# Kernel optimization log

Hardware: AMD Instinct MI355X
Metric: run time of the kernel (lower is better)

The kernel has to match this reference:

```python
import jax, jax.numpy as jnp
import numpy as np

N = 8192
C_IN = 512
C_INTER = 128  # in_channels // unit_nums = 512 // 4


def setup_inputs() -> dict:
    key = jax.random.key(0)
    ks = jax.random.split(key, 6)
    x = jax.random.normal(ks[0], (N, C_IN), dtype=jnp.float32)
    # Linear weights init: normal(0, 0.01); biases zero. Stored as [in, out].
    Wg = 0.01 * jax.random.normal(ks[1], (C_IN, C_INTER), dtype=jnp.float32)
    Wt = 0.01 * jax.random.normal(ks[2], (C_IN, C_INTER), dtype=jnp.float32)
    Wp = 0.01 * jax.random.normal(ks[3], (C_IN, C_INTER), dtype=jnp.float32)
    bg = jnp.zeros((C_INTER,), dtype=jnp.float32)
    bt = jnp.zeros((C_INTER,), dtype=jnp.float32)
    bp = jnp.zeros((C_INTER,), dtype=jnp.float32)
    # 1x1 conv weight (1, 2*C_INTER, 1, 1) flattened: first half hits theta, second half phi
    wcat = 0.01 * jax.random.normal(ks[4], (2 * C_INTER,), dtype=jnp.float32)
    return {"x": x, "Wg": Wg, "bg": bg, "Wt": Wt, "bt": bt, "Wp": Wp, "bp": bp, "wcat": wcat}


def reference(x, Wg, bg, Wt, bt, Wp, bp, wcat):
    n = x.shape[0]
    g_x = x @ Wg + bg          # [N, C_inter]
    theta = x @ Wt + bt        # [N, C_inter]
    phi = x @ Wp + bp          # [N, C_inter]
    c = theta.shape[1]
    # 1x1 conv over cat([theta_i, phi_j]) == w1.theta_i + w2.phi_j (outer sum), then ReLU
    a = theta @ wcat[:c]       # [N]
    b = phi @ wcat[c:]         # [N]
    f = jax.nn.relu(a[:, None] + b[None, :])  # [N, N]
    z = (f / n) @ g_x          # [N, C_inter]
    return z
```

## Files before the change

kernel.cpp:

```cpp
#include <hip/hip_runtime.h>

#define C_IN   512
#define C_INT  128
#define NBUCK  8192
#define SEG    32
#define NSEG   256

typedef short short8 __attribute__((ext_vector_type(8)));
typedef float floatx4 __attribute__((ext_vector_type(4)));


__device__ __forceinline__ int bucket_of(float v, float bmin, float inv_w) {
    float fk = (v - bmin) * inv_w;
    fk = fminf(fmaxf(fk, 0.f), (float)(NBUCK - 1));
    return (int)fk;
}

__device__ __forceinline__ short bf16rnd(float v) {
    unsigned u = __float_as_uint(v);
    return (short)((u + 0x7fffu + ((u >> 16) & 1u)) >> 16);
}


__global__ __launch_bounds__(256) void prep_kernel(
        const float* __restrict__ Wt, const float* __restrict__ Wp,
        const float* __restrict__ Wg, const float* __restrict__ wcat,
        const float* __restrict__ bt, const float* __restrict__ bp,
        float* __restrict__ ut, float* __restrict__ up, float* __restrict__ scal,
        unsigned short* __restrict__ WgT) {
    int t = threadIdx.x, bk = blockIdx.x;
    if (bk < 16) {
        const float* W  = (bk < 8) ? Wt : Wp;
        const float* wv = wcat + ((bk < 8) ? 0 : C_INT);
        float* dst      = (bk < 8) ? ut : up;
        int k = (bk & 7) * 64 + (t >> 2);
        int q = t & 3;
        const float4* row = (const float4*)(W + (size_t)k * C_INT);
        const float4* cv4 = (const float4*)wv;
        float s = 0.f;
        #pragma unroll
        for (int i = 0; i < 8; ++i) {
            float4 a = row[q * 8 + i];
            float4 c = cv4[q * 8 + i];
            s += a.x * c.x + a.y * c.y + a.z * c.z + a.w * c.w;
        }
        s += __shfl_xor(s, 1);
        s += __shfl_xor(s, 2);
        if (q == 0) dst[k] = s;
    } else if (bk == 16) {
        float sumsq = 0.f;
        const float4* w2v = (const float4*)(wcat + C_INT);
        for (int r = 0; r < 2; ++r) {
            int k = t * 2 + r;
            const float4* row = (const float4*)(Wp + (size_t)k * C_INT);
            float d = 0.f;
            #pragma unroll
            for (int i = 0; i < 32; ++i) {
                float4 a4 = row[i]; float4 c4 = w2v[i];
                d += a4.x * c4.x + a4.y * c4.y + a4.z * c4.z + a4.w * c4.w;
            }
            sumsq += d * d;
        }
        float s1p = (t < C_INT) ? bt[t] * wcat[t] : 0.f;
        float s2p = (t < C_INT) ? bp[t] * wcat[C_INT + t] : 0.f;
        for (int off = 32; off; off >>= 1) {
            s1p   += __shfl_down(s1p, off);
            s2p   += __shfl_down(s2p, off);
            sumsq += __shfl_down(sumsq, off);
        }
        __shared__ float red[12];
        int w = t >> 6, lane = t & 63;
        if (lane == 0) { red[w] = s1p; red[4 + w] = s2p; red[8 + w] = sumsq; }
        __syncthreads();
        if (t == 0) {
            float s0 = red[0] + red[1] + red[2] + red[3];
            float s1 = red[4] + red[5] + red[6] + red[7];
            float sq = red[8] + red[9] + red[10] + red[11];
            float sigma = sqrtf(sq);
            scal[0] = s0; scal[1] = s1;
            if (sigma > 1e-20f) {
                scal[2] = s1 - 8.f * sigma;
                scal[3] = (float)NBUCK / (16.f * sigma);
            } else {
                scal[2] = s1 - 1.f; scal[3] = 0.f;
            }
        }
    } else {
        __shared__ float tile[64][132];
        int kb = (bk - 17) * 64;
        #pragma unroll
        for (int it = 0; it < 8; ++it) {
            int idx = it * 256 + t;
            int r = idx >> 5, c4 = idx & 31;
            *(float4*)&tile[r][c4 * 4] =
                ((const float4*)(Wg + (size_t)(kb + r) * C_INT))[c4];
        }
        __syncthreads();
        int n = t & 127, kc = (t >> 7) * 32;
        unsigned pk[16];
        #pragma unroll
        for (int i = 0; i < 16; ++i) {
            unsigned lo = (unsigned short)bf16rnd(tile[kc + 2 * i][n]);
            unsigned hi = (unsigned short)bf16rnd(tile[kc + 2 * i + 1][n]);
            pk[i] = lo | (hi << 16);
        }
        uint4* dst = (uint4*)(WgT + (size_t)n * C_IN + kb + kc);
        #pragma unroll
        for (int i2 = 0; i2 < 4; ++i2) dst[i2] = *(uint4*)&pk[i2 * 4];
    }
}


#define RSTR 66

__global__ __launch_bounds__(256) void gemm_mfma(
        const float* __restrict__ x, const unsigned short* __restrict__ WgT,
        const float* __restrict__ bg,
        const float* __restrict__ ut, const float* __restrict__ up,
        const float* __restrict__ scal,
        _Float16* __restrict__ g, float* __restrict__ a, float* __restrict__ b) {
    __shared__ float red[3][36][RSTR];
    int tid = threadIdx.x;
    int lane = tid & 63, wv = tid >> 6;
    int i0 = blockIdx.x * 16;
    int m = lane & 15, q = lane >> 4;
    floatx4 accg[8] = {};
    floatx4 accab = {};
    const float* xrow = x + (size_t)(i0 + m) * C_IN + q * 8;
    const float* absrc = (m == 0) ? ut : up;
    #pragma unroll
    for (int ks = 0; ks < 4; ++ks) {
        int k0 = (wv * 4 + ks) * 32;
        float4 f0 = *(const float4*)(xrow + k0);
        float4 f1 = *(const float4*)(xrow + k0 + 4);
        short8 af;
        af[0] = bf16rnd(f0.x); af[1] = bf16rnd(f0.y);
        af[2] = bf16rnd(f0.z); af[3] = bf16rnd(f0.w);
        af[4] = bf16rnd(f1.x); af[5] = bf16rnd(f1.y);
        af[6] = bf16rnd(f1.z); af[7] = bf16rnd(f1.w);
        short8 abf = {};
        if (m < 2) {
            float4 u0 = *(const float4*)(absrc + k0 + q * 8);
            float4 u1 = *(const float4*)(absrc + k0 + q * 8 + 4);
            abf[0] = bf16rnd(u0.x); abf[1] = bf16rnd(u0.y);
            abf[2] = bf16rnd(u0.z); abf[3] = bf16rnd(u0.w);
            abf[4] = bf16rnd(u1.x); abf[5] = bf16rnd(u1.y);
            abf[6] = bf16rnd(u1.z); abf[7] = bf16rnd(u1.w);
        }
        accab = __builtin_amdgcn_mfma_f32_16x16x32_bf16(af, abf, accab, 0, 0, 0);
        #pragma unroll
        for (int f = 0; f < 8; ++f) {
            short8 bfr = *(const short8*)(WgT + (size_t)(f * 16 + m) * C_IN + k0 + q * 8);
            accg[f] = __builtin_amdgcn_mfma_f32_16x16x32_bf16(af, bfr, accg[f], 0, 0, 0);
        }
    }
    if (wv) {
        #pragma unroll
        for (int f = 0; f < 8; ++f)
            #pragma unroll
            for (int r = 0; r < 4; ++r)
                red[wv - 1][f * 4 + r][lane] = accg[f][r];
        #pragma unroll
        for (int r = 0; r < 4; ++r)
            red[wv - 1][32 + r][lane] = accab[r];
    }
    __syncthreads();
    if (wv == 0) {
        #pragma unroll
        for (int w = 0; w < 3; ++w) {
            #pragma unroll
            for (int f = 0; f < 8; ++f)
                #pragma unroll
                for (int r = 0; r < 4; ++r)
                    accg[f][r] += red[w][f * 4 + r][lane];
            #pragma unroll
            for (int r = 0; r < 4; ++r)
                accab[r] += red[w][32 + r][lane];
        }
        #pragma unroll
        for (int f = 0; f < 8; ++f) {
            int col = f * 16 + m;
            float bgv = bg[col];
            #pragma unroll
            for (int r = 0; r < 4; ++r) {
                int row = i0 + q * 4 + r;
                g[(size_t)row * C_INT + col] = (_Float16)(accg[f][r] + bgv);
            }
        }
        if (m < 2) {
            float off = m ? scal[1] : scal[0];
            float* dst = m ? b : a;
            #pragma unroll
            for (int r = 0; r < 4; ++r) dst[i0 + q * 4 + r] = accab[r] + off;
        }
    }
}


__global__ __launch_bounds__(1024) void sort_kernel(
        const float* __restrict__ b, const float* __restrict__ scal,
        unsigned* __restrict__ offs_g, unsigned short* __restrict__ perm_g,
        float* __restrict__ bsort_g) {
    __shared__ unsigned oh[NBUCK / 2];
    __shared__ unsigned cur[NBUCK / 2];
    __shared__ unsigned short ls[8192];
    __shared__ unsigned wtu[16];
    int t = threadIdx.x, lane = t & 63, wv = t >> 6;
    #pragma unroll
    for (int r = 0; r < 4; ++r) { oh[t + r * 1024] = 0u; cur[t + r * 1024] = 0u; }
    __syncthreads();
    float bmin = scal[2], inv_w = scal[3];
    int kb[8];
    #pragma unroll
    for (int r = 0; r < 8; ++r) {
        int j = t + r * 1024;
        kb[r] = bucket_of(b[j], bmin, inv_w);
        atomicAdd(&oh[kb[r] >> 1], (kb[r] & 1) ? 0x10000u : 1u);
    }
    __syncthreads();
    unsigned h[8], p = 0;
    #pragma unroll
    for (int w = 0; w < 4; ++w) {
        unsigned word = oh[t * 4 + w];
        p += word & 0xffffu;  h[w * 2]     = p;
        p += word >> 16;      h[w * 2 + 1] = p;
    }
    unsigned v = p;
    #pragma unroll
    for (int d = 1; d < 64; d <<= 1) {
        unsigned u = __shfl_up(v, d);
        if (lane >= d) v += u;
    }
    if (lane == 63) wtu[wv] = v;
    __syncthreads();
    if (t < 16) {
        unsigned w = wtu[t];
        #pragma unroll
        for (int d = 1; d < 16; d <<= 1) {
            unsigned u = __shfl_up(w, d);
            if (t >= d) w += u;
        }
        wtu[t] = w;
    }
    __syncthreads();
    unsigned base = (v - p) + (wv ? wtu[wv - 1] : 0u);
    #pragma unroll
    for (int w = 0; w < 4; ++w) {
        unsigned lo = base + h[w * 2], hi = base + h[w * 2 + 1];
        oh[t * 4 + w] = lo | (hi << 16);
        offs_g[t * 8 + w * 2 + 1] = lo;
        offs_g[t * 8 + w * 2 + 2] = hi;
    }
    if (t == 0) offs_g[0] = 0u;
    __syncthreads();
    #pragma unroll
    for (int r = 0; r < 8; ++r) {
        int j = t + r * 1024;
        int k = kb[r];
        unsigned st = 0u;
        if (k > 0) {
            unsigned word = oh[(k - 1) >> 1];
            st = ((k - 1) & 1) ? (word >> 16) : (word & 0xffffu);
        }
        unsigned old = atomicAdd(&cur[k >> 1], (k & 1) ? 0x10000u : 1u);
        unsigned pos = (k & 1) ? (old >> 16) : (old & 0xffffu);
        ls[st + pos] = (unsigned short)j;
    }
    __syncthreads();
    #pragma unroll
    for (int r = 0; r < 8; ++r) {
        int e = t + r * 1024;
        int j = ls[e];
        perm_g[e] = (unsigned short)j;
        bsort_g[e] = b[j];
    }
}


__global__ __launch_bounds__(128) void segsum_kernel(
        const _Float16* __restrict__ g, const unsigned short* __restrict__ perm,
        const float* __restrict__ bsort,
        float* __restrict__ seg1, float* __restrict__ seg2) {
    __shared__ int pj[SEG];
    __shared__ float pb[SEG];
    int s = blockIdx.x, t = threadIdx.x;
    if (t < SEG) { pj[t] = perm[s * SEG + t]; pb[t] = bsort[s * SEG + t]; }
    __syncthreads();
    float a1 = 0.f, a2 = 0.f;
    #pragma unroll
    for (int e = 0; e < SEG; ++e) {
        float gv = (float)g[(size_t)pj[e] * C_INT + t];
        a1 += gv; a2 += pb[e] * gv;
    }
    seg1[s * C_INT + t] = a1;
    seg2[s * C_INT + t] = a2;
}


__global__ __launch_bounds__(128) void expand_kernel(
        const _Float16* __restrict__ g, const unsigned short* __restrict__ perm,
        const float* __restrict__ bsort,
        const float* __restrict__ seg1, const float* __restrict__ seg2,
        float* __restrict__ Pr1, float* __restrict__ Pr2) {
    __shared__ int pj[SEG];
    __shared__ float pb[SEG];
    int s = blockIdx.x, t = threadIdx.x;
    if (t < SEG) { pj[t] = perm[s * SEG + t]; pb[t] = bsort[s * SEG + t]; }
    __syncthreads();
    float r1 = 0.f, r2 = 0.f;
    for (int s2 = s + 1; s2 < NSEG; ++s2) {
        r1 += seg1[s2 * C_INT + t];
        r2 += seg2[s2 * C_INT + t];
    }
    #pragma unroll
    for (int e = SEG - 1; e >= 0; --e) {
        float gv = (float)g[(size_t)pj[e] * C_INT + t];
        r1 += gv; r2 += pb[e] * gv;
        size_t idx = (size_t)(s * SEG + e) * C_INT + t;
        Pr1[idx] = r1; Pr2[idx] = r2;
    }
    if (s == NSEG - 1) {
        Pr1[(size_t)8192 * C_INT + t] = 0.f;
        Pr2[(size_t)8192 * C_INT + t] = 0.f;
    }
}


__global__ __launch_bounds__(128) void out_kernel(
        const float* __restrict__ a, const float* __restrict__ scal,
        const _Float16* __restrict__ g,
        const unsigned* __restrict__ offs, const unsigned short* __restrict__ perm,
        const float* __restrict__ bsort,
        const float* __restrict__ Pr1, const float* __restrict__ Pr2,
        float* __restrict__ out, float inv_n) {
    __shared__ int pj[128];
    __shared__ float pb[128];
    int i = blockIdx.x, c = threadIdx.x;
    float ai = a[i], thr = -ai;
    float bmin = scal[2], inv_w = scal[3];
    int ki = bucket_of(thr, bmin, inv_w);
    unsigned e0 = offs[ki], e1 = offs[ki + 1];
    size_t base = (size_t)e1 * C_INT + c;
    float acc = ai * Pr1[base] + Pr2[base];
    for (unsigned be = e0; be < e1; be += 128) {
        unsigned cnt = min(128u, e1 - be);
        if ((unsigned)c < cnt) { pj[c] = perm[be + c]; pb[c] = bsort[be + c]; }
        __syncthreads();
        for (unsigned r = 0; r < cnt; ++r) {
            float bj = pb[r];
            if (bj > thr)
                acc += (ai + bj) * (float)g[(size_t)pj[r] * C_INT + c];
        }
        __syncthreads();
    }
    out[(size_t)i * C_INT + c] = acc * inv_n;
}


extern "C" void kernel_launch(void* const* d_in, const int* in_sizes, int n_in,
                              void* d_out, int out_size, void* d_ws, size_t ws_size,
                              hipStream_t stream) {
    const float* x    = (const float*)d_in[0];
    const float* Wg   = (const float*)d_in[1];
    const float* bg   = (const float*)d_in[2];
    const float* Wt   = (const float*)d_in[3];
    const float* bt   = (const float*)d_in[4];
    const float* Wp   = (const float*)d_in[5];
    const float* bp   = (const float*)d_in[6];
    const float* wcat = (const float*)d_in[7];
    float* out = (float*)d_out;
    int n = in_sizes[0] / C_IN;

    char* w = (char*)d_ws;
    size_t off = 0;
    auto alloc = [&](size_t bytes) -> void* {
        void* p = w + off;
        off += (bytes + 255) & ~(size_t)255;
        return p;
    };
    float*          ut    = (float*)alloc(C_IN * 4);
    float*          up    = (float*)alloc(C_IN * 4);
    float*          scal  = (float*)alloc(16);
    float*          a     = (float*)alloc((size_t)n * 4);
    float*          b     = (float*)alloc((size_t)n * 4);
    unsigned*       offs  = (unsigned*)alloc((size_t)(NBUCK + 1) * 4);
    unsigned short* perm  = (unsigned short*)alloc((size_t)n * 2);
    float*          bsort = (float*)alloc((size_t)n * 4);
    _Float16*       g     = (_Float16*)alloc((size_t)n * C_INT * 2);
    unsigned short* WgT   = (unsigned short*)alloc((size_t)C_INT * C_IN * 2);
    float*          seg1  = (float*)alloc((size_t)NSEG * C_INT * 4);
    float*          seg2  = (float*)alloc((size_t)NSEG * C_INT * 4);
    float*          Pr1   = (float*)alloc((size_t)(n + 1) * C_INT * 4);
    float*          Pr2   = (float*)alloc((size_t)(n + 1) * C_INT * 4);

    prep_kernel<<<25, 256, 0, stream>>>(Wt, Wp, Wg, wcat, bt, bp, ut, up, scal, WgT);
    gemm_mfma<<<n / 16, 256, 0, stream>>>(x, WgT, bg, ut, up, scal, g, a, b);
    sort_kernel<<<1, 1024, 0, stream>>>(b, scal, offs, perm, bsort);
    segsum_kernel<<<NSEG, 128, 0, stream>>>(g, perm, bsort, seg1, seg2);
    expand_kernel<<<NSEG, 128, 0, stream>>>(g, perm, bsort, seg1, seg2, Pr1, Pr2);
    out_kernel<<<n, 128, 0, stream>>>(a, scal, g, offs, perm, bsort, Pr1, Pr2,
                                      out, 1.0f / (float)n);
}
```

Before: 151.8 us.

## Drop prefix-expansion kernel; sum segment totals and scan partial segment in output kernel

Removes the kernel that materialised full per-element suffix sums, avoiding writing and reading two N×C_INT float arrays. The output kernel instead sums coarse segment totals from the threshold segment onward and explicitly processes elements up to the segment boundary. Segment size grows to 128, so each output row now does extra gathered work over up to a full segment plus a loop over up to 64 segment totals.

```diff
diff --git a/kernel.cpp b/kernel.cpp
--- a/kernel.cpp
+++ b/kernel.cpp
@@ -3,8 +3,8 @@
 #define C_IN   512
 #define C_INT  128
 #define NBUCK  8192
-#define SEG    32
-#define NSEG   256
+#define SEG    128
+#define NSEG   64
 
 typedef short short8 __attribute__((ext_vector_type(8)));
 typedef float floatx4 __attribute__((ext_vector_type(4)));
@@ -284,45 +284,17 @@
     __shared__ int pj[SEG];
     __shared__ float pb[SEG];
     int s = blockIdx.x, t = threadIdx.x;
-    if (t < SEG) { pj[t] = perm[s * SEG + t]; pb[t] = bsort[s * SEG + t]; }
+    pj[t] = perm[s * SEG + t];
+    pb[t] = bsort[s * SEG + t];
     __syncthreads();
     float a1 = 0.f, a2 = 0.f;
-    #pragma unroll
+    #pragma unroll 8
     for (int e = 0; e < SEG; ++e) {
         float gv = (float)g[(size_t)pj[e] * C_INT + t];
         a1 += gv; a2 += pb[e] * gv;
     }
     seg1[s * C_INT + t] = a1;
     seg2[s * C_INT + t] = a2;
-}
-
-
-__global__ __launch_bounds__(128) void expand_kernel(
-        const _Float16* __restrict__ g, const unsigned short* __restrict__ perm,
-        const float* __restrict__ bsort,
-        const float* __restrict__ seg1, const float* __restrict__ seg2,
-        float* __restrict__ Pr1, float* __restrict__ Pr2) {
-    __shared__ int pj[SEG];
-    __shared__ float pb[SEG];
-    int s = blockIdx.x, t = threadIdx.x;
-    if (t < SEG) { pj[t] = perm[s * SEG + t]; pb[t] = bsort[s * SEG + t]; }
-    __syncthreads();
-    float r1 = 0.f, r2 = 0.f;
-    for (int s2 = s + 1; s2 < NSEG; ++s2) {
-        r1 += seg1[s2 * C_INT + t];
-        r2 += seg2[s2 * C_INT + t];
-    }
-    #pragma unroll
-    for (int e = SEG - 1; e >= 0; --e) {
-        float gv = (float)g[(size_t)pj[e] * C_INT + t];
-        r1 += gv; r2 += pb[e] * gv;
-        size_t idx = (size_t)(s * SEG + e) * C_INT + t;
-        Pr1[idx] = r1; Pr2[idx] = r2;
-    }
-    if (s == NSEG - 1) {
-        Pr1[(size_t)8192 * C_INT + t] = 0.f;
-        Pr2[(size_t)8192 * C_INT + t] = 0.f;
-    }
 }
 
 
@@ -331,7 +303,7 @@
         const _Float16* __restrict__ g,
         const unsigned* __restrict__ offs, const unsigned short* __restrict__ perm,
         const float* __restrict__ bsort,
-        const float* __restrict__ Pr1, const float* __restrict__ Pr2,
+        const float* __restrict__ seg1, const float* __restrict__ seg2,
         float* __restrict__ out, float inv_n) {
     __shared__ int pj[128];
     __shared__ float pb[128];
@@ -340,10 +312,16 @@
     float bmin = scal[2], inv_w = scal[3];
     int ki = bucket_of(thr, bmin, inv_w);
     unsigned e0 = offs[ki], e1 = offs[ki + 1];
-    size_t base = (size_t)e1 * C_INT + c;
-    float acc = ai * Pr1[base] + Pr2[base];
-    for (unsigned be = e0; be < e1; be += 128) {
-        unsigned cnt = min(128u, e1 - be);
+    unsigned sstar = (e1 + SEG - 1) / SEG;
+    float r1 = 0.f, r2 = 0.f;
+    for (unsigned s = sstar; s < NSEG; ++s) {
+        r1 += seg1[s * C_INT + c];
+        r2 += seg2[s * C_INT + c];
+    }
+    float acc = ai * r1 + r2;
+    unsigned eEnd = sstar * SEG;
+    for (unsigned be = e0; be < eEnd; be += 128) {
+        unsigned cnt = min(128u, eEnd - be);
         if ((unsigned)c < cnt) { pj[c] = perm[be + c]; pb[c] = bsort[be + c]; }
         __syncthreads();
         for (unsigned r = 0; r < cnt; ++r) {
@@ -390,14 +368,11 @@
     unsigned short* WgT   = (unsigned short*)alloc((size_t)C_INT * C_IN * 2);
     float*          seg1  = (float*)alloc((size_t)NSEG * C_INT * 4);
     float*          seg2  = (float*)alloc((size_t)NSEG * C_INT * 4);
-    float*          Pr1   = (float*)alloc((size_t)(n + 1) * C_INT * 4);
-    float*          Pr2   = (float*)alloc((size_t)(n + 1) * C_INT * 4);
 
     prep_kernel<<<25, 256, 0, stream>>>(Wt, Wp, Wg, wcat, bt, bp, ut, up, scal, WgT);
     gemm_mfma<<<n / 16, 256, 0, stream>>>(x, WgT, bg, ut, up, scal, g, a, b);
     sort_kernel<<<1, 1024, 0, stream>>>(b, scal, offs, perm, bsort);
     segsum_kernel<<<NSEG, 128, 0, stream>>>(g, perm, bsort, seg1, seg2);
-    expand_kernel<<<NSEG, 128, 0, stream>>>(g, perm, bsort, seg1, seg2, Pr1, Pr2);
-    out_kernel<<<n, 128, 0, stream>>>(a, scal, g, offs, perm, bsort, Pr1, Pr2,
+    out_kernel<<<n, 128, 0, stream>>>(a, scal, g, offs, perm, bsort, seg1, seg2,
                                       out, 1.0f / (float)n);
 }
```

After: 180.3 us. +18.8%, slower.

## Split GEMM output columns across two blocks and compute bucket range from data

Applied to the files above, without the earlier changes.

The projection GEMM grid is doubled so that each block computes half of the 128 g columns for a 16-row tile, which raises block count and lowers per-block register and shared-memory use. The bucket range for the counting sort is no longer estimated from a Wp-derived sigma in prep_kernel. Instead the sort kernel computes the true min and max of b and stores them for out_kernel. This removes the serial per-row dot-product loop in prep_kernel and gives buckets that fit the data, at the cost of an extra reduction in the single-block sort and reloading the x tile in both column-group blocks.

```diff
diff --git a/kernel.cpp b/kernel.cpp
--- a/kernel.cpp
+++ b/kernel.cpp
@@ -48,42 +48,19 @@
         s += __shfl_xor(s, 2);
         if (q == 0) dst[k] = s;
     } else if (bk == 16) {
-        float sumsq = 0.f;
-        const float4* w2v = (const float4*)(wcat + C_INT);
-        for (int r = 0; r < 2; ++r) {
-            int k = t * 2 + r;
-            const float4* row = (const float4*)(Wp + (size_t)k * C_INT);
-            float d = 0.f;
-            #pragma unroll
-            for (int i = 0; i < 32; ++i) {
-                float4 a4 = row[i]; float4 c4 = w2v[i];
-                d += a4.x * c4.x + a4.y * c4.y + a4.z * c4.z + a4.w * c4.w;
-            }
-            sumsq += d * d;
-        }
         float s1p = (t < C_INT) ? bt[t] * wcat[t] : 0.f;
         float s2p = (t < C_INT) ? bp[t] * wcat[C_INT + t] : 0.f;
         for (int off = 32; off; off >>= 1) {
-            s1p   += __shfl_down(s1p, off);
-            s2p   += __shfl_down(s2p, off);
-            sumsq += __shfl_down(sumsq, off);
-        }
-        __shared__ float red[12];
+            s1p += __shfl_down(s1p, off);
+            s2p += __shfl_down(s2p, off);
+        }
+        __shared__ float red[8];
         int w = t >> 6, lane = t & 63;
-        if (lane == 0) { red[w] = s1p; red[4 + w] = s2p; red[8 + w] = sumsq; }
+        if (lane == 0) { red[w] = s1p; red[4 + w] = s2p; }
         __syncthreads();
         if (t == 0) {
-            float s0 = red[0] + red[1] + red[2] + red[3];
-            float s1 = red[4] + red[5] + red[6] + red[7];
-            float sq = red[8] + red[9] + red[10] + red[11];
-            float sigma = sqrtf(sq);
-            scal[0] = s0; scal[1] = s1;
-            if (sigma > 1e-20f) {
-                scal[2] = s1 - 8.f * sigma;
-                scal[3] = (float)NBUCK / (16.f * sigma);
-            } else {
-                scal[2] = s1 - 1.f; scal[3] = 0.f;
-            }
+            scal[0] = red[0] + red[1] + red[2] + red[3];
+            scal[1] = red[4] + red[5] + red[6] + red[7];
         }
     } else {
         __shared__ float tile[64][132];
@@ -119,12 +96,14 @@
         const float* __restrict__ ut, const float* __restrict__ up,
         const float* __restrict__ scal,
         _Float16* __restrict__ g, float* __restrict__ a, float* __restrict__ b) {
-    __shared__ float red[3][36][RSTR];
+    __shared__ float red[3][20][RSTR];
     int tid = threadIdx.x;
     int lane = tid & 63, wv = tid >> 6;
-    int i0 = blockIdx.x * 16;
+    int bx = blockIdx.x;
+    int i0 = (bx >> 1) * 16;
+    int cg = bx & 1;
     int m = lane & 15, q = lane >> 4;
-    floatx4 accg[8] = {};
+    floatx4 accg[4] = {};
     floatx4 accab = {};
     const float* xrow = x + (size_t)(i0 + m) * C_IN + q * 8;
     const float* absrc = (m == 0) ? ut : up;
@@ -138,48 +117,50 @@
         af[2] = bf16rnd(f0.z); af[3] = bf16rnd(f0.w);
         af[4] = bf16rnd(f1.x); af[5] = bf16rnd(f1.y);
         af[6] = bf16rnd(f1.z); af[7] = bf16rnd(f1.w);
-        short8 abf = {};
-        if (m < 2) {
-            float4 u0 = *(const float4*)(absrc + k0 + q * 8);
-            float4 u1 = *(const float4*)(absrc + k0 + q * 8 + 4);
-            abf[0] = bf16rnd(u0.x); abf[1] = bf16rnd(u0.y);
-            abf[2] = bf16rnd(u0.z); abf[3] = bf16rnd(u0.w);
-            abf[4] = bf16rnd(u1.x); abf[5] = bf16rnd(u1.y);
-            abf[6] = bf16rnd(u1.z); abf[7] = bf16rnd(u1.w);
-        }
-        accab = __builtin_amdgcn_mfma_f32_16x16x32_bf16(af, abf, accab, 0, 0, 0);
-        #pragma unroll
-        for (int f = 0; f < 8; ++f) {
-            short8 bfr = *(const short8*)(WgT + (size_t)(f * 16 + m) * C_IN + k0 + q * 8);
+        if (cg == 0) {
+            short8 abf = {};
+            if (m < 2) {
+                float4 u0 = *(const float4*)(absrc + k0 + q * 8);
+                float4 u1 = *(const float4*)(absrc + k0 + q * 8 + 4);
+                abf[0] = bf16rnd(u0.x); abf[1] = bf16rnd(u0.y);
+                abf[2] = bf16rnd(u0.z); abf[3] = bf16rnd(u0.w);
+                abf[4] = bf16rnd(u1.x); abf[5] = bf16rnd(u1.y);
+                abf[6] = bf16rnd(u1.z); abf[7] = bf16rnd(u1.w);
+            }
+            accab = __builtin_amdgcn_mfma_f32_16x16x32_bf16(af, abf, accab, 0, 0, 0);
+        }
+        #pragma unroll
+        for (int f = 0; f < 4; ++f) {
+            short8 bfr = *(const short8*)(WgT + (size_t)(cg * 64 + f * 16 + m) * C_IN + k0 + q * 8);
             accg[f] = __builtin_amdgcn_mfma_f32_16x16x32_bf16(af, bfr, accg[f], 0, 0, 0);
         }
     }
     if (wv) {
         #pragma unroll
-        for (int f = 0; f < 8; ++f)
+        for (int f = 0; f < 4; ++f)
             #pragma unroll
             for (int r = 0; r < 4; ++r)
                 red[wv - 1][f * 4 + r][lane] = accg[f][r];
         #pragma unroll
         for (int r = 0; r < 4; ++r)
-            red[wv - 1][32 + r][lane] = accab[r];
+            red[wv - 1][16 + r][lane] = accab[r];
     }
     __syncthreads();
     if (wv == 0) {
         #pragma unroll
         for (int w = 0; w < 3; ++w) {
             #pragma unroll
-            for (int f = 0; f < 8; ++f)
+            for (int f = 0; f < 4; ++f)
                 #pragma unroll
                 for (int r = 0; r < 4; ++r)
                     accg[f][r] += red[w][f * 4 + r][lane];
             #pragma unroll
             for (int r = 0; r < 4; ++r)
-                accab[r] += red[w][32 + r][lane];
-        }
-        #pragma unroll
-        for (int f = 0; f < 8; ++f) {
-            int col = f * 16 + m;
+                accab[r] += red[w][16 + r][lane];
+        }
+        #pragma unroll
+        for (int f = 0; f < 4; ++f) {
+            int col = cg * 64 + f * 16 + m;
             float bgv = bg[col];
             #pragma unroll
             for (int r = 0; r < 4; ++r) {
@@ -187,7 +168,7 @@
                 g[(size_t)row * C_INT + col] = (_Float16)(accg[f][r] + bgv);
             }
         }
-        if (m < 2) {
+        if (cg == 0 && m < 2) {
             float off = m ? scal[1] : scal[0];
             float* dst = m ? b : a;
             #pragma unroll
@@ -198,23 +179,47 @@
 
 
 __global__ __launch_bounds__(1024) void sort_kernel(
-        const float* __restrict__ b, const float* __restrict__ scal,
+        const float* __restrict__ b, float* __restrict__ scal,
         unsigned* __restrict__ offs_g, unsigned short* __restrict__ perm_g,
         float* __restrict__ bsort_g) {
     __shared__ unsigned oh[NBUCK / 2];
     __shared__ unsigned cur[NBUCK / 2];
     __shared__ unsigned short ls[8192];
     __shared__ unsigned wtu[16];
+    __shared__ float smn[16], smx[16], sbp[2];
     int t = threadIdx.x, lane = t & 63, wv = t >> 6;
     #pragma unroll
     for (int r = 0; r < 4; ++r) { oh[t + r * 1024] = 0u; cur[t + r * 1024] = 0u; }
-    __syncthreads();
-    float bmin = scal[2], inv_w = scal[3];
+    float bv[8];
+    float mn = 1e30f, mx = -1e30f;
+    #pragma unroll
+    for (int r = 0; r < 8; ++r) {
+        bv[r] = b[t + r * 1024];
+        mn = fminf(mn, bv[r]); mx = fmaxf(mx, bv[r]);
+    }
+    for (int off = 32; off; off >>= 1) {
+        mn = fminf(mn, __shfl_down(mn, off));
+        mx = fmaxf(mx, __shfl_down(mx, off));
+    }
+    if (lane == 0) { smn[wv] = mn; smx[wv] = mx; }
+    __syncthreads();
+    if (t == 0) {
+        float gmn = smn[0], gmx = smx[0];
+        #pragma unroll
+        for (int i = 1; i < 16; ++i) {
+            gmn = fminf(gmn, smn[i]); gmx = fmaxf(gmx, smx[i]);
+        }
+        float range = gmx - gmn;
+        float iw = (range > 1e-30f) ? (float)NBUCK / range : 0.f;
+        sbp[0] = gmn; sbp[1] = iw;
+        scal[4] = gmn; scal[5] = iw;
+    }
+    __syncthreads();
+    float bmin = sbp[0], inv_w = sbp[1];
     int kb[8];
     #pragma unroll
     for (int r = 0; r < 8; ++r) {
-        int j = t + r * 1024;
-        kb[r] = bucket_of(b[j], bmin, inv_w);
+        kb[r] = bucket_of(bv[r], bmin, inv_w);
         atomicAdd(&oh[kb[r] >> 1], (kb[r] & 1) ? 0x10000u : 1u);
     }
     __syncthreads();
@@ -337,7 +342,7 @@
     __shared__ float pb[128];
     int i = blockIdx.x, c = threadIdx.x;
     float ai = a[i], thr = -ai;
-    float bmin = scal[2], inv_w = scal[3];
+    float bmin = scal[4], inv_w = scal[5];
     int ki = bucket_of(thr, bmin, inv_w);
     unsigned e0 = offs[ki], e1 = offs[ki + 1];
     size_t base = (size_t)e1 * C_INT + c;
@@ -380,7 +385,7 @@
     };
     float*          ut    = (float*)alloc(C_IN * 4);
     float*          up    = (float*)alloc(C_IN * 4);
-    float*          scal  = (float*)alloc(16);
+    float*          scal  = (float*)alloc(32);
     float*          a     = (float*)alloc((size_t)n * 4);
     float*          b     = (float*)alloc((size_t)n * 4);
     unsigned*       offs  = (unsigned*)alloc((size_t)(NBUCK + 1) * 4);
@@ -394,7 +399,7 @@
     float*          Pr2   = (float*)alloc((size_t)(n + 1) * C_INT * 4);
 
     prep_kernel<<<25, 256, 0, stream>>>(Wt, Wp, Wg, wcat, bt, bp, ut, up, scal, WgT);
-    gemm_mfma<<<n / 16, 256, 0, stream>>>(x, WgT, bg, ut, up, scal, g, a, b);
+    gemm_mfma<<<n / 8, 256, 0, stream>>>(x, WgT, bg, ut, up, scal, g, a, b);
     sort_kernel<<<1, 1024, 0, stream>>>(b, scal, offs, perm, bsort);
     segsum_kernel<<<NSEG, 128, 0, stream>>>(g, perm, bsort, seg1, seg2);
     expand_kernel<<<NSEG, 128, 0, stream>>>(g, perm, bsort, seg1, seg2, Pr1, Pr2);
```

After: 142.7 us. -6.0%, faster.
